# Performance work log

Hardware: AMD Instinct MI355X
Metric: run time of the kernel (lower is better)

Reference implementation:

```python
import jax, jax.numpy as jnp
import numpy as np

B, N, DIM, H, DH, K = 4, 2048, 512, 6, 64, 16
KEEP_PROB = 0.9  # 1 - dropout_rate
LOG2PI = float(np.log(2.0 * np.pi))
LOG_PRIOR = float(np.log(1.0 / K))


def setup_inputs() -> dict:
    key = jax.random.key(0)
    ks = jax.random.split(key, 7)
    inputs_q = jax.random.normal(ks[0], (B, N, DIM), dtype=jnp.float32)
    # decoder-style causal mask, shape [B, 1, q_len, kv_len]
    causal = jnp.tril(jnp.ones((N, N), dtype=jnp.float32))
    mask = jnp.broadcast_to(causal[None, None], (B, 1, N, N))
    # dropout keep mask broadcast across the query dim: [B, H, 1, kv_len]
    keep = jax.random.bernoulli(ks[1], KEEP_PROB, (B, H, 1, N)).astype(jnp.float32)
    w_qkv = jax.random.normal(ks[2], (DIM, 3 * H * DH), dtype=jnp.float32) * 0.02
    w_out = jax.random.normal(ks[3], (H * DH, DIM), dtype=jnp.float32) * 0.02
    mu_lookup = jax.random.normal(ks[4], (K, DIM), dtype=jnp.float32)
    logvar_lookup = jax.random.normal(ks[5], (K, DIM), dtype=jnp.float32) * 0.1
    return {
        "inputs_q": inputs_q,
        "mask": mask,
        "keep": keep,
        "w_qkv": w_qkv,
        "w_out": w_out,
        "mu_lookup": mu_lookup,
        "logvar_lookup": logvar_lookup,
    }


def reference(inputs_q, mask, keep, w_qkv, w_out, mu_lookup, logvar_lookup):
    # --- MultiHeadDotProductAttention (self-attn path) ---
    qkv = (inputs_q @ w_qkv).reshape(B, N, 3, H, DH)  # [B,N,3,H,DH]
    q, k, v = qkv[:, :, 0], qkv[:, :, 1], qkv[:, :, 2]
    # bias: 0 where mask > 0, -1e10 elsewhere (note: no 1/sqrt(d) scaling, as in source)
    bias = jnp.where(mask > 0, 0.0, -1e10)
    attn_weights = jnp.einsum('bqhd,bkhd->bhqk', q, k) + bias  # [B,H,N,N]
    attn_weights = jax.nn.softmax(attn_weights, axis=-1)
    # broadcast dropout: mask shared across the query dim
    attn_weights = attn_weights * keep / KEEP_PROB
    attn_out = jnp.einsum('bhqk,bkhd->bqhd', attn_weights, v)
    attn_out = attn_out.reshape(B, N, H * DH) @ w_out  # [B,N,DIM]

    # --- GMM posterior approx q(y|x) ~= p(y|z) (approx_qy_x, vectorized over k) ---
    z = attn_out.mean(axis=1)  # pooled latent, [B,DIM]
    diff = z[:, None, :] - mu_lookup[None]  # [B,K,DIM]
    llh = -0.5 * jnp.sum(
        diff * diff / jnp.exp(logvar_lookup)[None] + logvar_lookup[None] + LOG2PI,
        axis=-1,
    )  # [B,K]
    logLogit_qy_x = llh + LOG_PRIOR
    qy_x = jax.nn.softmax(logLogit_qy_x, axis=1)  # [B,K]

    # combine mixture mean back in so both branches are live in one output
    return attn_out + (qy_x @ mu_lookup)[:, None, :]
```

## Files before the change

kernel.cpp:

```cpp
#include <hip/hip_runtime.h>
#include <hip/hip_cooperative_groups.h>
#include <cstdint>
#include <cstddef>

namespace cg = cooperative_groups;

#define NH 6
#define NSEQ 2048
#define DIMD 512
#define BATCH 4
#define HD 384
#define LOG2PI_F 1.8378770664093453f
#define LOG2E_F 1.4426950408889634f
#define M12L2_F (-17.312340490667562f)

typedef __attribute__((ext_vector_type(8))) short short8;
typedef __attribute__((ext_vector_type(8))) unsigned short ushort8;
typedef __attribute__((ext_vector_type(4))) unsigned short ushort4v;
typedef __attribute__((ext_vector_type(4))) float floatx4;

__device__ inline unsigned short f2bf(float f){
  unsigned int u = __float_as_uint(f);
  u += 0x7FFFu + ((u>>16)&1u);
  return (unsigned short)(u>>16);
}

__device__ inline float exp2_raw(float x){
  float r; asm("v_exp_f32 %0, %1" : "=v"(r) : "v"(x)); return r;
}

#define GLD16(gp, lp) __builtin_amdgcn_global_load_lds( \
  (const __attribute__((address_space(1))) void*)(gp), \
  (__attribute__((address_space(3))) void*)(lp), 16, 0, 0)

__device__ inline void wtrans_body(
    const float* __restrict__ src, unsigned short* __restrict__ dst,
    int R, int C, int bx, int by, unsigned short* Ls, int t)
{
  const int r = t>>2, c0 = (t&3)*16;
  const int d0 = by*64, n0 = bx*64;
  #pragma unroll
  for (int j=0;j<16;j+=4){
    floatx4 v = *(const floatx4*)(src + (size_t)(d0+r)*C + n0 + c0 + j);
    #pragma unroll
    for(int jj=0;jj<4;jj++) Ls[r*72 + c0+j+jj] = f2bf(v[jj]);
  }
  __syncthreads();
  #pragma unroll
  for (int j=0;j<16;j+=8){
    ushort8 o;
    #pragma unroll
    for(int jj=0;jj<8;jj++) o[jj] = Ls[(c0+j+jj)*72 + r];
    *(ushort8*)(dst + (size_t)(n0+r)*R + d0 + c0 + j) = o;
  }
}

__global__ __launch_bounds__(256) void prep(
    const float* __restrict__ xq, unsigned short* __restrict__ xbf,
    const float* __restrict__ w_qkv, unsigned short* __restrict__ wqT,
    const float* __restrict__ w_out, unsigned short* __restrict__ woT,
    float* __restrict__ z)
{
  __shared__ __attribute__((aligned(16))) unsigned short Ls[64*72];
  const int bid = blockIdx.x, t = threadIdx.x;
  if (bid < 4096){
    if (bid == 0){
      #pragma unroll
      for(int j=0;j<8;j++) z[t*8+j] = 0.f;
    }
    int i = bid*256 + t;
    floatx4 v = *(const floatx4*)(xq + (size_t)i*4);
    ushort4v r;
    #pragma unroll
    for(int j=0;j<4;j++) r[j] = f2bf(v[j]);
    *(ushort4v*)(xbf + (size_t)i*4) = r;
  } else if (bid < 4240){
    int rb = bid - 4096;
    wtrans_body(w_qkv, wqT, 512, 1152, rb%18, rb/18, Ls, t);
  } else {
    int rb = bid - 4240;
    wtrans_body(w_out, woT, 384, 512, rb%8, rb/8, Ls, t);
  }
}

__global__ __launch_bounds__(256) void gemm_qkv(
    const unsigned short* __restrict__ A,
    const unsigned short* __restrict__ Bt,
    const float* __restrict__ keep,
    unsigned short* __restrict__ Qo, unsigned short* __restrict__ Ko,
    unsigned short* __restrict__ Vt)
{
  __shared__ __attribute__((aligned(16))) unsigned short Cs[128*132];
  unsigned short* As = Cs;
  unsigned short* Bs = Cs + 128*64;
  const int tid = threadIdx.x;
  const int w = tid>>6, lane = tid&63;
  const int wr = w>>1, wc = w&1;
  const int quad = lane>>4, l16 = lane&15;
  const int tM = blockIdx.x*128, tN = blockIdx.y*128;
  const int r8 = lane>>3, c8 = (lane&7)*8;
  floatx4 acc[4][4];
  floatx4 zed = {0.f,0.f,0.f,0.f};
  #pragma unroll
  for (int i=0;i<4;i++)
    #pragma unroll
    for(int j=0;j<4;j++) acc[i][j] = zed;

  for (int k0=0; k0<512; k0+=64){
    #pragma unroll
    for (int i=0;i<4;i++){
      int row = w*32 + i*8;
      GLD16(A  + (size_t)(tM+row+r8)*512 + k0 + c8, As + row*64);
      GLD16(Bt + (size_t)(tN+row+r8)*512 + k0 + c8, Bs + row*64);
    }
    __syncthreads();
    #pragma unroll
    for (int kk=0; kk<64; kk+=32){
      short8 af[4], bf[4];
      #pragma unroll
      for(int mt=0;mt<4;mt++)
        af[mt] = *(const short8*)(As + (wr*64+mt*16+l16)*64 + kk + quad*8);
      #pragma unroll
      for(int nt=0;nt<4;nt++)
        bf[nt] = *(const short8*)(Bs + (wc*64+nt*16+l16)*64 + kk + quad*8);
      #pragma unroll
      for(int mt=0;mt<4;mt++)
        #pragma unroll
        for(int nt=0;nt<4;nt++)
          acc[mt][nt] = __builtin_amdgcn_mfma_f32_16x16x32_bf16(af[mt], bf[nt], acc[mt][nt], 0,0,0);
    }
    __syncthreads();
  }
  #pragma unroll
  for(int mt=0;mt<4;mt++)
    #pragma unroll
    for(int nt=0;nt<4;nt++){
      int gcol = tN + wc*64 + nt*16 + l16;
      float qs = (gcol < 384) ? LOG2E_F : 1.0f;
      #pragma unroll
      for(int r=0;r<4;r++)
        Cs[(wr*64+mt*16+quad*4+r)*132 + wc*64+nt*16+l16] = f2bf(acc[mt][nt][r]*qs);
    }
  __syncthreads();
  if (blockIdx.y < 6){
    const int row = tid>>1, colh = (tid&1)*64;
    const int gcol0 = tN + colh;
    const int t = gcol0/384, rem = gcol0 - t*384, h = rem>>6;
    const int grow = tM + row, b = grow>>11, n = grow & 2047;
    unsigned short* dst = (t==0 ? Qo : Ko) + ((size_t)((b*NH+h)*NSEQ+n))*64;
    #pragma unroll
    for(int j=0;j<8;j++)
      *(ushort8*)(dst + j*8) = *(const ushort8*)(Cs + row*132 + colh + j*8);
  } else {
    const int dcol = tid>>1;
    const int nh   = (tid&1)*64;
    const int gcol = tN + dcol;
    const int rem = gcol - 768, h = rem>>6, dh = rem&63;
    const int b = tM>>11, nb = tM & 2047;
    const float* kp = keep + (size_t)(b*NH+h)*NSEQ + nb + nh;
    unsigned short* dst = Vt + ((size_t)((b*NH+h)*64 + dh))*NSEQ + nb + nh;
    #pragma unroll
    for (int j8=0;j8<8;j8++){
      floatx4 k0 = *(const floatx4*)(kp + j8*8);
      floatx4 k1 = *(const floatx4*)(kp + j8*8 + 4);
      ushort8 o;
      #pragma unroll
      for(int u=0;u<4;u++)
        o[u]   = (k0[u] < 0.5f) ? (unsigned short)0 : Cs[(nh + j8*8 + u)*132 + dcol];
      #pragma unroll
      for(int u=0;u<4;u++)
        o[4+u] = (k1[u] < 0.5f) ? (unsigned short)0 : Cs[(nh + j8*8 + 4 + u)*132 + dcol];
      *(ushort8*)(dst + j8*8) = o;
    }
  }
}

__global__ __launch_bounds__(256, 3) void attn_kernel(
    const unsigned short* __restrict__ Qg, const unsigned short* __restrict__ Kg,
    const unsigned short* __restrict__ VtG,
    unsigned short* __restrict__ atp)
{
  __shared__ __attribute__((aligned(16))) float sm[4*32*34 + 128];
  float* Ocs  = sm;
  float* accs = sm + 4*32*34;
  const int tid = threadIdx.x;
  const int w = tid>>6, lane = tid&63;
  const int quad = lane>>4, l16 = lane&15;
  const int bid = blockIdx.x;
  const int idx = bid>>3;
  const int bh  = (bid&7) + 8*(idx % 3);
  const int c   = 63 - idx/3;
  const int b = bh/NH, h = bh - b*NH;
  const unsigned short* Qb = Qg  + (size_t)bh*NSEQ*64;
  const int q0 = c*32;
  const int nkt = (c>>1) + 1;
  const int q_abs0 = q0 + l16;

  const unsigned short* Kl = Kg  + (size_t)bh*NSEQ*64 + (size_t)l16*64 + quad*8;
  const unsigned short* Vl = VtG + (size_t)bh*64*NSEQ + (size_t)l16*NSEQ + quad*8;

  short8 qf[2][2];
  #pragma unroll
  for(int mt=0;mt<2;mt++)
    #pragma unroll
    for(int kc=0;kc<2;kc++)
      qf[mt][kc] = *(const short8*)(Qb + (size_t)(q0+mt*16+l16)*64 + kc*32 + quad*8);

  floatx4 O[2][4];
  float accl[2] = {0.f, 0.f};
  floatx4 zed = {0.f,0.f,0.f,0.f};
  floatx4 m12v = {M12L2_F, M12L2_F, M12L2_F, M12L2_F};
  #pragma unroll
  for(int mt=0;mt<2;mt++)
    #pragma unroll
    for(int dt=0;dt<4;dt++) O[mt][dt] = zed;

  for (int kt = w; kt < nkt; kt += 4){
    const int kB = kt*64;
    short8 vf[2][4];
    const unsigned short* vp0 = Vl + kB;
    #pragma unroll
    for(int kh=0;kh<2;kh++)
      #pragma unroll
      for(int dt=0;dt<4;dt++)
        vf[kh][dt] = *(const short8*)(vp0 + (size_t)dt*32768 + kh*32);

    floatx4 sacc[2][4];
    #pragma unroll
    for(int mt=0;mt<2;mt++)
      #pragma unroll
      for(int nt=0;nt<4;nt++) sacc[mt][nt] = m12v;
    const unsigned short* kp0 = Kl + (size_t)kt*4096;
    #pragma unroll
    for(int nt=0;nt<4;nt++){
      short8 kf0 = *(const short8*)(kp0 + nt*1024);
      short8 kf1 = *(const short8*)(kp0 + nt*1024 + 32);
      #pragma unroll
      for(int mt=0;mt<2;mt++){
        sacc[mt][nt] = __builtin_amdgcn_mfma_f32_16x16x32_bf16(kf0, qf[mt][0], sacc[mt][nt], 0,0,0);
        sacc[mt][nt] = __builtin_amdgcn_mfma_f32_16x16x32_bf16(kf1, qf[mt][1], sacc[mt][nt], 0,0,0);
      }
    }

    const bool dia = (kt == nkt-1);
    #pragma unroll
    for(int mt=0;mt<2;mt++){
      const int qa = q_abs0 + mt*16;
      unsigned int d0[4], d1[4];
      float rs = 0.f;
      #pragma unroll
      for(int nt=0;nt<4;nt++){
        const int key0 = kB + nt*16 + quad*4;
        float p0 = exp2_raw(sacc[mt][nt][0]);
        float p1 = exp2_raw(sacc[mt][nt][1]);
        float p2 = exp2_raw(sacc[mt][nt][2]);
        float p3 = exp2_raw(sacc[mt][nt][3]);
        if (dia){
          p0 = (key0   <= qa) ? p0 : 0.f;
          p1 = (key0+1 <= qa) ? p1 : 0.f;
          p2 = (key0+2 <= qa) ? p2 : 0.f;
          p3 = (key0+3 <= qa) ? p3 : 0.f;
        }
        rs += (p0+p1) + (p2+p3);
        asm("v_cvt_pk_bf16_f32 %0, %1, %2" : "=v"(d0[nt]) : "v"(p0), "v"(p1));
        asm("v_cvt_pk_bf16_f32 %0, %1, %2" : "=v"(d1[nt]) : "v"(p2), "v"(p3));
      }
      accl[mt] += rs;
      #pragma unroll
      for(int kh=0;kh<2;kh++){
        unsigned int x0 = d0[2*kh],   x1 = d1[2*kh];
        unsigned int y0 = d0[2*kh+1], y1 = d1[2*kh+1];
        asm("v_permlane32_swap_b32 %0, %1" : "+v"(x0), "+v"(y0));
        asm("v_permlane16_swap_b32 %0, %1" : "+v"(x0), "+v"(y0));
        asm("v_permlane32_swap_b32 %0, %1" : "+v"(x1), "+v"(y1));
        asm("v_permlane16_swap_b32 %0, %1" : "+v"(x1), "+v"(y1));
        union { unsigned int u[4]; short8 s; } cvt;
        cvt.u[0] = x0; cvt.u[1] = x1; cvt.u[2] = y0; cvt.u[3] = y1;
        short8 pf = cvt.s;
        #pragma unroll
        for(int dt=0;dt<4;dt++)
          O[mt][dt] = __builtin_amdgcn_mfma_f32_16x16x32_bf16(pf, vf[kh][dt], O[mt][dt], 0,0,0);
      }
    }
  }

  #pragma unroll
  for(int mt=0;mt<2;mt++){
    accl[mt] += __shfl_xor(accl[mt], 16, 64);
    accl[mt] += __shfl_xor(accl[mt], 32, 64);
  }
  if (quad == 0){
    accs[w*32 + l16]      = accl[0];
    accs[w*32 + 16 + l16] = accl[1];
  }

  const int orow = tid>>3, oc4 = (tid&7)*4;
  float sc2 = 0.f;
  #pragma unroll
  for (int h2=0; h2<2; ++h2){
    float* Ow = Ocs + w*(32*34);
    #pragma unroll
    for(int mt=0;mt<2;mt++)
      #pragma unroll
      for(int d2=0;d2<2;d2++){
        const int dt = h2*2 + d2;
        #pragma unroll
        for(int r=0;r<4;r++)
          Ow[(mt*16+quad*4+r)*34 + d2*16 + l16] = O[mt][dt][r];
      }
    __syncthreads();
    if (h2 == 0){
      float as = accs[orow] + accs[32+orow] + accs[64+orow] + accs[96+orow];
      sc2 = (1.0f/0.9f) / as;
    }
    float fv[4];
    #pragma unroll
    for(int j=0;j<4;j++) fv[j] = 0.f;
    #pragma unroll
    for(int s=0;s<4;s++){
      const float* p = Ocs + s*(32*34) + orow*34 + oc4;
      #pragma unroll
      for(int j=0;j<4;j++) fv[j] += p[j];
    }
    ushort4v o4;
    #pragma unroll
    for(int j=0;j<4;j++) o4[j] = f2bf(fv[j]*sc2);
    *(ushort4v*)(atp + ((size_t)(b*NSEQ + q0 + orow))*HD + h*64 + h2*32 + oc4) = o4;
    __syncthreads();
  }
}

__global__ __launch_bounds__(256) void proj_gmm(
    const unsigned short* __restrict__ A,
    const unsigned short* __restrict__ Bt,
    const float* __restrict__ mu,
    const float* __restrict__ lv,
    float* __restrict__ out,
    float* __restrict__ z)
{
  __shared__ __attribute__((aligned(16))) unsigned short As[128*64];
  __shared__ __attribute__((aligned(16))) unsigned short Bs[128*64];
  __shared__ float sh[16];
  __shared__ float qy[16];
  const int tid = threadIdx.x;
  const int w = tid>>6, lane = tid&63;
  const int wr = w>>1, wc = w&1;
  const int quad = lane>>4, l16 = lane&15;
  const int tM = blockIdx.x*128, tN = blockIdx.y*128;
  const int r8 = lane>>3, c8 = (lane&7)*8;
  floatx4 acc[4][4];
  floatx4 zed = {0.f,0.f,0.f,0.f};
  #pragma unroll
  for (int i=0;i<4;i++)
    #pragma unroll
    for(int j=0;j<4;j++) acc[i][j] = zed;

  for (int k0=0; k0<384; k0+=64){
    #pragma unroll
    for (int i=0;i<4;i++){
      int row = w*32 + i*8;
      GLD16(A  + (size_t)(tM+row+r8)*384 + k0 + c8, As + row*64);
      GLD16(Bt + (size_t)(tN+row+r8)*384 + k0 + c8, Bs + row*64);
    }
    __syncthreads();
    #pragma unroll
    for (int kk=0; kk<64; kk+=32){
      short8 af[4], bf[4];
      #pragma unroll
      for(int mt=0;mt<4;mt++)
        af[mt] = *(const short8*)(As + (wr*64+mt*16+l16)*64 + kk + quad*8);
      #pragma unroll
      for(int nt=0;nt<4;nt++)
        bf[nt] = *(const short8*)(Bs + (wc*64+nt*16+l16)*64 + kk + quad*8);
      #pragma unroll
      for(int mt=0;mt<4;mt++)
        #pragma unroll
        for(int nt=0;nt<4;nt++)
          acc[mt][nt] = __builtin_amdgcn_mfma_f32_16x16x32_bf16(af[mt], bf[nt], acc[mt][nt], 0,0,0);
    }
    __syncthreads();
  }

  const int bq = tM>>11;
  #pragma unroll
  for(int nt=0;nt<4;nt++){
    float s = 0.f;
    #pragma unroll
    for(int mt=0;mt<4;mt++)
      #pragma unroll
      for(int r=0;r<4;r++) s += acc[mt][nt][r];
    s += __shfl_xor(s, 16, 64);
    s += __shfl_xor(s, 32, 64);
    if (quad == 0){
      int gcol = tN + wc*64 + nt*16 + l16;
      atomicAdd(&z[bq*DIMD + gcol], s);
    }
  }

  cg::this_grid().sync();

  {
    const int k = tid>>4, li = tid&15;
    float part = 0.f;
    for(int d=li; d<DIMD; d+=16){
      float zz = z[bq*DIMD+d] * (1.0f/2048.0f);
      float m = mu[k*DIMD+d], l = lv[k*DIMD+d];
      float diff = zz - m;
      part += diff*diff*__expf(-l) + l + LOG2PI_F;
    }
    #pragma unroll
    for(int off=8;off>=1;off>>=1) part += __shfl_xor(part, off, 64);
    if (li==0) sh[k] = part;
  }
  __syncthreads();
  if (tid<16){
    float logit = -0.5f*sh[tid];
    float mx = logit;
    #pragma unroll
    for(int off=8;off>=1;off>>=1) mx = fmaxf(mx, __shfl_xor(mx, off, 64));
    float e = __expf(logit-mx);
    float se = e;
    #pragma unroll
    for(int off=8;off>=1;off>>=1) se += __shfl_xor(se, off, 64);
    qy[tid] = e/se;
  }
  __syncthreads();

  #pragma unroll
  for(int nt=0;nt<4;nt++){
    const int gcol = tN + wc*64 + nt*16 + l16;
    float cc = 0.f;
    #pragma unroll
    for(int kk=0;kk<16;kk++) cc += qy[kk]*mu[kk*DIMD+gcol];
    #pragma unroll
    for(int mt=0;mt<4;mt++){
      const int grow = tM + wr*64 + mt*16 + quad*4;
      #pragma unroll
      for(int r=0;r<4;r++)
        out[(size_t)(grow+r)*512 + gcol] = acc[mt][nt][r] + cc;
    }
  }
}

extern "C" void kernel_launch(void* const* d_in, const int* in_sizes, int n_in,
                              void* d_out, int out_size, void* d_ws, size_t ws_size,
                              hipStream_t stream) {
  const float* inputs_q = (const float*)d_in[0];
  const float* keep  = (const float*)d_in[2];
  const float* w_qkv = (const float*)d_in[3];
  const float* w_out = (const float*)d_in[4];
  const float* mu    = (const float*)d_in[5];
  const float* lv    = (const float*)d_in[6];
  float* out = (float*)d_out;
  char* ws = (char*)d_ws;
  size_t off = 0;
  auto alloc = [&](size_t bytes){ void* p = ws + off; off += (bytes + 255) & ~(size_t)255; return p; };
  unsigned short* Qb  = (unsigned short*)alloc((size_t)24*2048*64*2);
  unsigned short* Kb  = (unsigned short*)alloc((size_t)24*2048*64*2);
  unsigned short* Vt  = (unsigned short*)alloc((size_t)24*64*2048*2);
  unsigned short* xbf = (unsigned short*)alloc((size_t)8192*512*2);
  unsigned short* wqT = (unsigned short*)alloc((size_t)1152*512*2);
  unsigned short* woT = (unsigned short*)alloc((size_t)512*384*2);
  unsigned short* atp = (unsigned short*)alloc((size_t)8192*384*2);
  float* z  = (float*)alloc((size_t)4*512*4);

  prep<<<4288, 256, 0, stream>>>(inputs_q, xbf, w_qkv, wqT, w_out, woT, z);
  gemm_qkv<<<dim3(64,9), 256, 0, stream>>>(xbf, wqT, keep, Qb, Kb, Vt);
  attn_kernel<<<1536, 256, 0, stream>>>(Qb, Kb, Vt, atp);

  const unsigned short* atp_c = atp;
  const unsigned short* woT_c = woT;
  void* args[] = { (void*)&atp_c, (void*)&woT_c, (void*)&mu, (void*)&lv,
                   (void*)&out, (void*)&z };
  hipLaunchCooperativeKernel((void*)proj_gmm, dim3(64,4), dim3(256),
                             args, 0, stream);
}
```

Measured before the change: 254.2 us.

## Split cooperative proj+GMM kernel into GEMM and separate GMM-add kernel

Replaces the cooperative launch with its grid-wide sync by two ordinary kernels. The first does the output projection, writes the result and accumulates the pooled sums. The second computes the GMM posterior per batch and adds the mixture mean to the output in place, using vectorized accesses. This removes the cooperative-launch and grid-barrier overhead, but adds one more launch and an extra read and write pass over the full 16 MB output.

```diff
diff --git a/kernel.cpp b/kernel.cpp
--- a/kernel.cpp
+++ b/kernel.cpp
@@ -1,9 +1,6 @@
 #include <hip/hip_runtime.h>
-#include <hip/hip_cooperative_groups.h>
 #include <cstdint>
 #include <cstddef>
-
-namespace cg = cooperative_groups;
 
 #define NH 6
 #define NSEQ 2048
@@ -330,18 +327,14 @@
   }
 }
 
-__global__ __launch_bounds__(256) void proj_gmm(
+__global__ __launch_bounds__(256) void gemm_proj(
     const unsigned short* __restrict__ A,
     const unsigned short* __restrict__ Bt,
-    const float* __restrict__ mu,
-    const float* __restrict__ lv,
     float* __restrict__ out,
     float* __restrict__ z)
 {
   __shared__ __attribute__((aligned(16))) unsigned short As[128*64];
   __shared__ __attribute__((aligned(16))) unsigned short Bs[128*64];
-  __shared__ float sh[16];
-  __shared__ float qy[16];
   const int tid = threadIdx.x;
   const int w = tid>>6, lane = tid&63;
   const int wr = w>>1, wc = w&1;
@@ -380,8 +373,17 @@
     }
     __syncthreads();
   }
-
-  const int bq = tM>>11;
+  #pragma unroll
+  for(int mt=0;mt<4;mt++){
+    int grow = tM + wr*64 + mt*16 + quad*4;
+    #pragma unroll
+    for(int nt=0;nt<4;nt++){
+      int gcol = tN + wc*64 + nt*16 + l16;
+      #pragma unroll
+      for(int r=0;r<4;r++)
+        out[(size_t)(grow+r)*512 + gcol] = acc[mt][nt][r];
+    }
+  }
   #pragma unroll
   for(int nt=0;nt<4;nt++){
     float s = 0.f;
@@ -393,17 +395,24 @@
     s += __shfl_xor(s, 32, 64);
     if (quad == 0){
       int gcol = tN + wc*64 + nt*16 + l16;
-      atomicAdd(&z[bq*DIMD + gcol], s);
-    }
-  }
-
-  cg::this_grid().sync();
-
+      atomicAdd(&z[(tM>>11)*DIMD + gcol], s);
+    }
+  }
+}
+
+__global__ __launch_bounds__(256) void gmm_add(
+    const float* __restrict__ z, const float* __restrict__ mu,
+    const float* __restrict__ lv, float* __restrict__ out)
+{
+  __shared__ float sh[16];
+  __shared__ float qy[16];
+  const int tid = threadIdx.x, bid = blockIdx.x;
+  const int b = bid>>6;
   {
     const int k = tid>>4, li = tid&15;
     float part = 0.f;
     for(int d=li; d<DIMD; d+=16){
-      float zz = z[bq*DIMD+d] * (1.0f/2048.0f);
+      float zz = z[b*DIMD+d] * (1.0f/2048.0f);
       float m = mu[k*DIMD+d], l = lv[k*DIMD+d];
       float diff = zz - m;
       part += diff*diff*__expf(-l) + l + LOG2PI_F;
@@ -426,19 +435,22 @@
   }
   __syncthreads();
 
-  #pragma unroll
-  for(int nt=0;nt<4;nt++){
-    const int gcol = tN + wc*64 + nt*16 + l16;
-    float cc = 0.f;
-    #pragma unroll
-    for(int kk=0;kk<16;kk++) cc += qy[kk]*mu[kk*DIMD+gcol];
-    #pragma unroll
-    for(int mt=0;mt<4;mt++){
-      const int grow = tM + wr*64 + mt*16 + quad*4;
-      #pragma unroll
-      for(int r=0;r<4;r++)
-        out[(size_t)(grow+r)*512 + gcol] = acc[mt][nt][r] + cc;
-    }
+  const int col4 = (tid&127)*4;
+  const int rhalf = tid>>7;
+  floatx4 cc = {0.f,0.f,0.f,0.f};
+  #pragma unroll
+  for(int kk=0;kk<16;kk++){
+    const float q = qy[kk];
+    const float* mp = mu + kk*DIMD + col4;
+    cc[0] += q*mp[0]; cc[1] += q*mp[1]; cc[2] += q*mp[2]; cc[3] += q*mp[3];
+  }
+  float* ob = out + (size_t)bid*32*DIMD + rhalf*DIMD + col4;
+  #pragma unroll
+  for(int r=0;r<16;r++){
+    float* p = ob + (size_t)r*2*DIMD;
+    floatx4 a = *(const floatx4*)p;
+    a[0]+=cc[0]; a[1]+=cc[1]; a[2]+=cc[2]; a[3]+=cc[3];
+    *(floatx4*)p = a;
   }
 }
 
@@ -467,11 +479,6 @@
   prep<<<4288, 256, 0, stream>>>(inputs_q, xbf, w_qkv, wqT, w_out, woT, z);
   gemm_qkv<<<dim3(64,9), 256, 0, stream>>>(xbf, wqT, keep, Qb, Kb, Vt);
   attn_kernel<<<1536, 256, 0, stream>>>(Qb, Kb, Vt, atp);
-
-  const unsigned short* atp_c = atp;
-  const unsigned short* woT_c = woT;
-  void* args[] = { (void*)&atp_c, (void*)&woT_c, (void*)&mu, (void*)&lv,
-                   (void*)&out, (void*)&z };
-  hipLaunchCooperativeKernel((void*)proj_gmm, dim3(64,4), dim3(256),
-                             args, 0, stream);
-}
+  gemm_proj<<<dim3(64,4), 256, 0, stream>>>(atp, woT, out, z);
+  gmm_add<<<256, 256, 0, stream>>>(z, mu, lv, out);
+}
```

Result: faster. 227.4 us (median of 2 runs) (-10.5%).
